# Kernel tuning notes

Hardware: AMD Instinct MI355X
Metric: run time of the kernel (lower is better)

## Reference

```python
import jax, jax.numpy as jnp
import numpy as np

N_NODES = 100000
N_EDGES = 1600000
N_PAIRS = 500000
IN_C, HID_C, OUT_C = 128, 128, 128


def setup_inputs() -> dict:
    key = jax.random.key(0)
    ks = jax.random.split(key, 12)
    def lin(k, fan_in, shape):
        b = 1.0 / np.sqrt(fan_in)
        return jax.random.uniform(k, shape, jnp.float32, -b, b)
    return {
        "x": jax.random.normal(ks[0], (N_NODES, IN_C), jnp.float32),
        "edge_index": jax.random.randint(ks[1], (2, N_EDGES), 0, N_NODES),
        "edge_pairs": jax.random.randint(ks[2], (2, N_PAIRS), 0, N_NODES),
        "W1": lin(ks[3], IN_C, (IN_C, HID_C)),
        "b1": jnp.zeros((HID_C,), jnp.float32),
        "W2": lin(ks[4], HID_C, (HID_C, OUT_C)),
        "b2": jnp.zeros((OUT_C,), jnp.float32),
        "Wm1": lin(ks[5], 2 * OUT_C, (2 * OUT_C, HID_C)),
        "bm1": lin(ks[6], 2 * OUT_C, (HID_C,)),
        "Wm2": lin(ks[7], HID_C, (HID_C, 1)),
        "bm2": lin(ks[8], HID_C, (1,)),
    }


def reference(x, edge_index, edge_pairs, W1, b1, W2, b2, Wm1, bm1, Wm2, bm2):
    N = x.shape[0]
    loop = jnp.arange(N, dtype=edge_index.dtype)
    row = jnp.concatenate([edge_index[0], loop])  # source nodes (+self loops)
    col = jnp.concatenate([edge_index[1], loop])  # target nodes (+self loops)
    # symmetric GCN normalization: deg^{-1/2}[row] * deg^{-1/2}[col]
    deg = jax.ops.segment_sum(jnp.ones(col.shape, x.dtype), col, num_segments=N)
    dinv = jnp.where(deg > 0, jax.lax.rsqrt(deg), 0.0)
    norm = dinv[row] * dinv[col]  # [E+N]

    def gcn_conv(h, W, b):
        h = h @ W  # transform first (PyG GCNConv lin has no bias)
        msg = h[row] * norm[:, None]
        return jax.ops.segment_sum(msg, col, num_segments=N) + b

    h = jax.nn.relu(gcn_conv(x, W1, b1))
    h = gcn_conv(h, W2, b2)  # dropout p=0.0 -> identity

    src, dst = edge_pairs[0], edge_pairs[1]
    ef = jnp.concatenate([h[src], h[dst]], axis=-1)  # [P, 2*out]
    out = jax.nn.relu(ef @ Wm1 + bm1) @ Wm2 + bm2
    return out.squeeze(-1)
```

## Files before the change

kernel.cpp:

```cpp
#include <hip/hip_runtime.h>
#include <hip/hip_fp16.h>

#define NCH 128
#define G_NODES 256
#define EPB 4096
#define RCAP 4864
#define MAXNB 512
#define KST 40

typedef __attribute__((ext_vector_type(8))) short short8;
typedef _Float16 half8 __attribute__((ext_vector_type(8)));
typedef __attribute__((ext_vector_type(4))) float floatx4;

static inline size_t align256(size_t x){ return (x + 255) & ~(size_t)255; }

__global__ __launch_bounds__(256) void binA_kernel(
    const int* __restrict__ row, const int* __restrict__ col,
    int* __restrict__ gcur, unsigned* __restrict__ bucketed, int E, int NB){
  __shared__ int cnt[MAXNB];
  __shared__ int lbase[MAXNB];
  __shared__ int gbase[MAXNB];
  __shared__ unsigned sorted[EPB];
  __shared__ unsigned short binOf[EPB];
  __shared__ int sh[256];
  __shared__ int carry;
  int t = threadIdx.x;
  int e0 = blockIdx.x * EPB;
  int ecnt = min(EPB, E - e0);
  for (int i = t; i < NB; i += 256) cnt[i] = 0;
  if (t == 0) carry = 0;
  __syncthreads();
  unsigned rec[16]; int bn[16]; int rk[16];
  #pragma unroll
  for (int i = 0; i < 16; i++){
    int e = e0 + i * 256 + t;
    if (e < E){
      int r = row[e], c = col[e];
      bn[i]  = c >> 8;
      rec[i] = (unsigned)r | ((unsigned)(c & 255) << 17);
      rk[i]  = atomicAdd(&cnt[bn[i]], 1);
    } else bn[i] = -1;
  }
  __syncthreads();
  for (int start = 0; start < NB; start += 256){
    int i = start + t;
    int v = (i < NB) ? cnt[i] : 0;
    sh[t] = v; __syncthreads();
    for (int off = 1; off < 256; off <<= 1){
      int val = (t >= off) ? sh[t - off] : 0;
      __syncthreads(); sh[t] += val; __syncthreads();
    }
    if (i < NB) lbase[i] = sh[t] - v + carry;
    __syncthreads();
    if (t == 255) carry += sh[255];
    __syncthreads();
  }
  for (int i = t; i < NB; i += 256){
    int c = cnt[i];
    gbase[i] = (c > 0) ? atomicAdd(&gcur[i], c) : 0;
  }
  __syncthreads();
  #pragma unroll
  for (int i = 0; i < 16; i++){
    if (bn[i] >= 0){
      int pos = lbase[bn[i]] + rk[i];
      sorted[pos] = rec[i];
      binOf[pos]  = (unsigned short)bn[i];
    }
  }
  __syncthreads();
  for (int idx = t; idx < ecnt; idx += 256){
    int b = binOf[idx];
    int gpos = gbase[b] + (idx - lbase[b]);
    if (gpos < RCAP) bucketed[(size_t)b * RCAP + gpos] = sorted[idx];
  }
}

__global__ void bscan_kernel(const int* __restrict__ gcur, int* __restrict__ bbase, int nb){
  __shared__ int sh[256];
  __shared__ int carry;
  int t = threadIdx.x;
  if (t == 0) carry = 0;
  __syncthreads();
  for (int start = 0; start < nb; start += 256){
    int i = start + t;
    int v = (i < nb) ? min(gcur[i], RCAP) : 0;
    int orig = v;
    sh[t] = v; __syncthreads();
    for (int off = 1; off < 256; off <<= 1){
      int val = (t >= off) ? sh[t - off] : 0;
      __syncthreads(); sh[t] += val; __syncthreads();
    }
    if (i < nb) bbase[i] = sh[t] - orig + carry;
    __syncthreads();
    if (t == 255) carry += sh[255];
    __syncthreads();
  }
}

__global__ __launch_bounds__(256) void binB_kernel(
    const unsigned* __restrict__ bucketed, const int* __restrict__ gcur,
    const int* __restrict__ bbase, int* __restrict__ rows_sorted,
    int* __restrict__ offs, int* __restrict__ counts, float* __restrict__ dinv, int N){
  __shared__ unsigned ledge[RCAP];
  __shared__ int cnt[G_NODES];
  __shared__ int cnt2[G_NODES];
  __shared__ int lex[G_NODES];
  __shared__ int sh[256];
  int b = blockIdx.x, t = threadIdx.x;
  int size = min(gcur[b], RCAP);
  int base = bbase[b];
  int n0 = b * G_NODES;
  cnt[t] = 0; cnt2[t] = 0;
  __syncthreads();
  for (int i = t; i < size; i += 256){
    unsigned v = bucketed[(size_t)b * RCAP + i];
    ledge[i] = v;
    atomicAdd(&cnt[v >> 17], 1);
  }
  __syncthreads();
  {
    int v = cnt[t];
    sh[t] = v; __syncthreads();
    for (int off = 1; off < 256; off <<= 1){
      int val = (t >= off) ? sh[t - off] : 0;
      __syncthreads(); sh[t] += val; __syncthreads();
    }
    lex[t] = sh[t] - v;
    int n = n0 + t;
    if (n < N){
      counts[n] = v;
      offs[n]   = base + sh[t] - v;
      dinv[n]   = rsqrtf((float)v + 1.0f);
    }
  }
  __syncthreads();
  for (int i = t; i < size; i += 256){
    unsigned v = ledge[i];
    int node = v >> 17;
    int pos = lex[node] + atomicAdd(&cnt2[node], 1);
    rows_sorted[base + pos] = (int)(v & 0x1FFFFu);
  }
}

__global__ void wprep_kernel(const float* __restrict__ W1, const float* __restrict__ W2,
                             const float* __restrict__ Wm1, short* __restrict__ planes){
  int mat = blockIdx.x >> 6;
  int idx = ((blockIdx.x & 63) << 8) + threadIdx.x;
  int k = idx >> 7, n = idx & 127;
  const float* src = (mat == 0) ? W1 : (mat == 1) ? W2 : (mat == 2) ? Wm1 : (Wm1 + 16384);
  float x = src[idx];
  short hs, ls;
  if (mat == 0){
    unsigned u = __float_as_uint(x);
    hs = (short)(u >> 16);
    float hf = __uint_as_float(u & 0xFFFF0000u);
    ls = (short)(__float_as_uint(x - hf) >> 16);
  } else {
    __half h = __float2half(x);
    __half l = __float2half(x - __half2float(h));
    hs = __half_as_short(h); ls = __half_as_short(l);
  }
  planes[(size_t)(2 * mat) * 16384 + n * 128 + k]     = hs;
  planes[(size_t)(2 * mat + 1) * 16384 + n * 128 + k] = ls;
}

__global__ __launch_bounds__(512, 4) void gemm_f32(
    const float* __restrict__ X, const short* __restrict__ Whi_,
    const short* __restrict__ Wlo_, const float* __restrict__ scale,
    __half* __restrict__ O, int nrows, int do_scale){
  __shared__ short Xhi[128 * KST];
  __shared__ short Xlo[128 * KST];
  __shared__ short Whi[128 * KST];
  __shared__ short Wlo[128 * KST];
  int t = threadIdx.x;
  int w = t >> 6, lane = t & 63;
  int m = lane & 15, q = lane >> 4;
  int row0 = blockIdx.x * 128;
  floatx4 acc[8];
  #pragma unroll
  for (int ct = 0; ct < 8; ct++) acc[ct] = (floatx4)0.f;

  for (int kc = 0; kc < 4; kc++){
    int k0 = kc * 32;
    __syncthreads();
    #pragma unroll
    for (int qq = 0; qq < 2; qq++){
      int f = t + 512 * qq;
      int r = f >> 3, kq = f & 7;
      int gr = row0 + r;
      int grc = (gr < nrows) ? gr : 0;
      float4 v = *(const float4*)(X + (size_t)grc * NCH + k0 + kq * 4);
      short h[4], l[4];
      float vv[4] = {v.x, v.y, v.z, v.w};
      #pragma unroll
      for (int j = 0; j < 4; j++){
        unsigned u = __float_as_uint(vv[j]);
        h[j] = (short)(u >> 16);
        float hf = __uint_as_float(u & 0xFFFF0000u);
        l[j] = (short)(__float_as_uint(vv[j] - hf) >> 16);
      }
      *(uint2*)(Xhi + r * KST + kq * 4) = *(uint2*)h;
      *(uint2*)(Xlo + r * KST + kq * 4) = *(uint2*)l;
    }
    {
      int n = t >> 2, kq = t & 3;
      *(uint4*)(Whi + n * KST + kq * 8) = *(const uint4*)(Whi_ + n * NCH + k0 + kq * 8);
      *(uint4*)(Wlo + n * KST + kq * 8) = *(const uint4*)(Wlo_ + n * NCH + k0 + kq * 8);
    }
    __syncthreads();
    short8 a_hi = *(const short8*)(Xhi + (w * 16 + m) * KST + q * 8);
    short8 a_lo = *(const short8*)(Xlo + (w * 16 + m) * KST + q * 8);
    #pragma unroll
    for (int ct = 0; ct < 8; ct++){
      short8 b_hi = *(const short8*)(Whi + (ct * 16 + m) * KST + q * 8);
      short8 b_lo = *(const short8*)(Wlo + (ct * 16 + m) * KST + q * 8);
      acc[ct] = __builtin_amdgcn_mfma_f32_16x16x32_bf16(a_hi, b_hi, acc[ct], 0, 0, 0);
      acc[ct] = __builtin_amdgcn_mfma_f32_16x16x32_bf16(a_lo, b_hi, acc[ct], 0, 0, 0);
      acc[ct] = __builtin_amdgcn_mfma_f32_16x16x32_bf16(a_hi, b_lo, acc[ct], 0, 0, 0);
    }
  }
  #pragma unroll
  for (int r = 0; r < 4; r++){
    int grow = row0 + w * 16 + q * 4 + r;
    if (grow < nrows){
      float sc = do_scale ? scale[grow] : 1.0f;
      #pragma unroll
      for (int ct = 0; ct < 8; ct++)
        O[(size_t)grow * NCH + ct * 16 + m] = __float2half(acc[ct][r] * sc);
    }
  }
}

template<int NCT>
__global__ __launch_bounds__(512, 4) void gemm_f16k(
    const __half* __restrict__ X,
    const short* __restrict__ Whi0, const short* __restrict__ Wlo0,
    const short* __restrict__ Whi1, const short* __restrict__ Wlo1,
    const float* __restrict__ scale,
    __half* __restrict__ O0, __half* __restrict__ O1, int nrows, int do_scale){
  __shared__ short Xs[128 * KST];
  __shared__ short Whs[NCT * 16 * KST];
  __shared__ short Wls[NCT * 16 * KST];
  int t = threadIdx.x;
  int w = t >> 6, lane = t & 63;
  int m = lane & 15, q = lane >> 4;
  int row0 = blockIdx.x * 128;
  floatx4 acc[NCT];
  #pragma unroll
  for (int ct = 0; ct < NCT; ct++) acc[ct] = (floatx4)0.f;

  for (int kc = 0; kc < 4; kc++){
    int k0 = kc * 32;
    __syncthreads();
    {
      int r = t >> 2, kq = t & 3;
      int gr = row0 + r;
      int grc = (gr < nrows) ? gr : 0;
      *(uint4*)(Xs + r * KST + kq * 8) = *(const uint4*)(X + (size_t)grc * NCH + k0 + kq * 8);
    }
    #pragma unroll
    for (int i = t; i < NCT * 16 * 4; i += 512){
      int n = i >> 2, kq = i & 3;
      const short* sh = (n < 128) ? (Whi0 + n * NCH) : (Whi1 + (n - 128) * NCH);
      const short* sl = (n < 128) ? (Wlo0 + n * NCH) : (Wlo1 + (n - 128) * NCH);
      *(uint4*)(Whs + n * KST + kq * 8) = *(const uint4*)(sh + k0 + kq * 8);
      *(uint4*)(Wls + n * KST + kq * 8) = *(const uint4*)(sl + k0 + kq * 8);
    }
    __syncthreads();
    half8 a = *(const half8*)(Xs + (w * 16 + m) * KST + q * 8);
    #pragma unroll
    for (int ct = 0; ct < NCT; ct++){
      half8 bh = *(const half8*)(Whs + (ct * 16 + m) * KST + q * 8);
      half8 bl = *(const half8*)(Wls + (ct * 16 + m) * KST + q * 8);
      acc[ct] = __builtin_amdgcn_mfma_f32_16x16x32_f16(a, bh, acc[ct], 0, 0, 0);
      acc[ct] = __builtin_amdgcn_mfma_f32_16x16x32_f16(a, bl, acc[ct], 0, 0, 0);
    }
  }
  #pragma unroll
  for (int r = 0; r < 4; r++){
    int grow = row0 + w * 16 + q * 4 + r;
    if (grow < nrows){
      float sc = do_scale ? scale[grow] : 1.0f;
      #pragma unroll
      for (int ct = 0; ct < NCT; ct++){
        __half val = __float2half(acc[ct][r] * sc);
        if (ct < 8) O0[(size_t)grow * NCH + ct * 16 + m] = val;
        else        O1[(size_t)grow * NCH + (ct - 8) * 16 + m] = val;
      }
    }
  }
}

__global__ __launch_bounds__(256) void agg_kernel(
    const __half* __restrict__ s, const float* __restrict__ dinv,
    const int* __restrict__ offs, const int* __restrict__ counts,
    const int* __restrict__ rows_sorted, const float* __restrict__ bias,
    __half* __restrict__ outp, int N, int do_relu){
  int wave = (int)((blockIdx.x * blockDim.x + threadIdx.x) >> 6);
  int lane = threadIdx.x & 63;
  if (wave >= N) return;
  int c = wave;
  int g = lane >> 4, h = lane & 15;
  float acc[8] = {0.f,0.f,0.f,0.f,0.f,0.f,0.f,0.f};
  if (g == 0){
    uint4 v = *(const uint4*)(s + (size_t)c * NCH + h * 8);
    const __half2* hp = (const __half2*)&v;
    #pragma unroll
    for (int i = 0; i < 4; i++){
      float2 f = __half22float2(hp[i]);
      acc[2*i] += f.x; acc[2*i+1] += f.y;
    }
  }
  int off = offs[c], cnt = counts[c];
  for (int chunk = 0; chunk < cnt; chunk += 64){
    int nn = min(64, cnt - chunk);
    int myidx = (lane < nn) ? rows_sorted[off + chunk + lane] : 0;
    int jmax = (nn + 3) >> 2;
    #pragma unroll 4
    for (int j = 0; j < jmax; j++){
      int e = 4 * j + g;
      int r = __shfl(myidx, e & 63, 64);
      if (e < nn){
        uint4 v = *(const uint4*)(s + (size_t)r * NCH + h * 8);
        const __half2* hp = (const __half2*)&v;
        #pragma unroll
        for (int i = 0; i < 4; i++){
          float2 f = __half22float2(hp[i]);
          acc[2*i] += f.x; acc[2*i+1] += f.y;
        }
      }
    }
  }
  #pragma unroll
  for (int i = 0; i < 8; i++){
    acc[i] += __shfl_xor(acc[i], 16, 64);
    acc[i] += __shfl_xor(acc[i], 32, 64);
  }
  if (g == 0){
    float di = dinv[c];
    float4 b0 = *(const float4*)(bias + h * 8);
    float4 b1 = *(const float4*)(bias + h * 8 + 4);
    float o[8];
    o[0] = di*acc[0]+b0.x; o[1] = di*acc[1]+b0.y; o[2] = di*acc[2]+b0.z; o[3] = di*acc[3]+b0.w;
    o[4] = di*acc[4]+b1.x; o[5] = di*acc[5]+b1.y; o[6] = di*acc[6]+b1.z; o[7] = di*acc[7]+b1.w;
    if (do_relu){
      #pragma unroll
      for (int i = 0; i < 8; i++) o[i] = fmaxf(o[i], 0.f);
    }
    __half2 packed[4];
    #pragma unroll
    for (int i = 0; i < 4; i++) packed[i] = __floats2half2_rn(o[2*i], o[2*i+1]);
    *(uint4*)(outp + (size_t)c * NCH + h * 8) = *(uint4*)packed;
  }
}

__global__ __launch_bounds__(256) void pair_kernel(
    const __half* __restrict__ A, const __half* __restrict__ B,
    const int* __restrict__ src, const int* __restrict__ dst,
    const float* __restrict__ bm1, const float* __restrict__ Wm2,
    const float* __restrict__ bm2, float* __restrict__ outp, int P){
  int gwave = (int)((blockIdx.x * blockDim.x + threadIdx.x) >> 6);
  int lane  = threadIdx.x & 63;
  int nw    = (int)((gridDim.x * blockDim.x) >> 6);
  int g = lane >> 4, h = lane & 15;
  float bb[8], ww[8];
  {
    float4 t0 = *(const float4*)(bm1 + h * 8);
    float4 t1 = *(const float4*)(bm1 + h * 8 + 4);
    bb[0]=t0.x; bb[1]=t0.y; bb[2]=t0.z; bb[3]=t0.w;
    bb[4]=t1.x; bb[5]=t1.y; bb[6]=t1.z; bb[7]=t1.w;
    float4 w0 = *(const float4*)(Wm2 + h * 8);
    float4 w1 = *(const float4*)(Wm2 + h * 8 + 4);
    ww[0]=w0.x; ww[1]=w0.y; ww[2]=w0.z; ww[3]=w0.w;
    ww[4]=w1.x; ww[5]=w1.y; ww[6]=w1.z; ww[7]=w1.w;
  }
  float bsc = bm2[0];
  const __half* basep = (g & 1) ? B : A;
  for (int p0 = gwave * 2; p0 < P; p0 += nw * 2){
    int pi = p0 + (g >> 1);
    int piX = (pi < P) ? pi : p0;
    int node = (g & 1) ? dst[piX] : src[piX];
    uint4 v = *(const uint4*)(basep + (size_t)node * NCH + h * 8);
    const __half2* hp = (const __half2*)&v;
    float f[8];
    #pragma unroll
    for (int i = 0; i < 4; i++){
      float2 t = __half22float2(hp[i]);
      f[2*i] = t.x; f[2*i+1] = t.y;
    }
    float partial = 0.f;
    #pragma unroll
    for (int i = 0; i < 8; i++){
      float other = __shfl_xor(f[i], 16, 64);
      float zi = fmaxf(f[i] + other + bb[i], 0.f);
      partial += zi * ww[i];
    }
    partial += __shfl_xor(partial, 1, 64);
    partial += __shfl_xor(partial, 2, 64);
    partial += __shfl_xor(partial, 4, 64);
    partial += __shfl_xor(partial, 8, 64);
    if ((lane & 31) == 0 && pi < P) outp[pi] = partial + bsc;
  }
}


extern "C" void kernel_launch(void* const* d_in, const int* in_sizes, int n_in,
                              void* d_out, int out_size, void* d_ws, size_t ws_size,
                              hipStream_t stream){
  const float* x   = (const float*)d_in[0];
  const int*   ei  = (const int*)  d_in[1];
  const int*   ep  = (const int*)  d_in[2];
  const float* W1  = (const float*)d_in[3];
  const float* b1  = (const float*)d_in[4];
  const float* W2  = (const float*)d_in[5];
  const float* b2  = (const float*)d_in[6];
  const float* Wm1 = (const float*)d_in[7];
  const float* bm1 = (const float*)d_in[8];
  const float* Wm2 = (const float*)d_in[9];
  const float* bm2 = (const float*)d_in[10];
  float* outp = (float*)d_out;

  const int N = in_sizes[0] / NCH;
  const int E = in_sizes[1] / 2;
  const int P = in_sizes[2] / 2;
  const int NB = (N + G_NODES - 1) / G_NODES;

  char* base = (char*)d_ws;
  size_t off = 0;
  int*      counts      = (int*)     (base + off); off = align256(off + (size_t)N * 4);
  int*      offs        = (int*)     (base + off); off = align256(off + (size_t)N * 4);
  float*    dinv        = (float*)   (base + off); off = align256(off + (size_t)N * 4);
  int*      gcur        = (int*)     (base + off); off = align256(off + (size_t)NB * 4);
  int*      bbase       = (int*)     (base + off); off = align256(off + (size_t)NB * 4);
  unsigned* bucketed    = (unsigned*)(base + off); off = align256(off + (size_t)NB * RCAP * 4);
  int*      rows_sorted = (int*)     (base + off); off = align256(off + (size_t)E * 4);
  short*    planes      = (short*)   (base + off); off = align256(off + (size_t)8 * 16384 * 2);
  __half*   sbuf        = (__half*)  (base + off); off = align256(off + (size_t)N * NCH * 2);
  __half*   hbuf        = (__half*)  (base + off); off = align256(off + (size_t)N * NCH * 2);
  __half*   sA          = (__half*)  (base + off); off = align256(off + (size_t)N * NCH * 2);
  __half*   sB          = (__half*)  (base + off); off = align256(off + (size_t)N * NCH * 2);
  (void)ws_size; (void)n_in; (void)out_size;

  short* W1hi = planes + 0 * 16384;
  short* W1lo = planes + 1 * 16384;
  short* W2hi = planes + 2 * 16384;
  short* W2lo = planes + 3 * 16384;
  short* Wahi = planes + 4 * 16384;
  short* Walo = planes + 5 * 16384;
  short* Wbhi = planes + 6 * 16384;
  short* Wblo = planes + 7 * 16384;

  const int* row = ei;
  const int* col = ei + E;
  const int* psrc = ep;
  const int* pdst = ep + P;

  hipMemsetAsync(gcur, 0, (size_t)NB * 4, stream);

  binA_kernel <<<(E + EPB - 1) / EPB, 256, 0, stream>>>(row, col, gcur, bucketed, E, NB);
  bscan_kernel<<<1, 256, 0, stream>>>(gcur, bbase, NB);
  binB_kernel <<<NB, 256, 0, stream>>>(bucketed, gcur, bbase, rows_sorted, offs, counts, dinv, N);
  wprep_kernel<<<256, 256, 0, stream>>>(W1, W2, Wm1, planes);

  int gemm_grid = (N + 127) / 128;
  int agg_grid  = (N + 3) / 4;

  gemm_f32<<<gemm_grid, 512, 0, stream>>>(x, W1hi, W1lo, dinv, sbuf, N, 1);
  agg_kernel<<<agg_grid, 256, 0, stream>>>(sbuf, dinv, offs, counts, rows_sorted, b1, hbuf, N, 1);
  gemm_f16k<8><<<gemm_grid, 512, 0, stream>>>(hbuf, W2hi, W2lo, W2hi, W2lo, dinv, sbuf, sbuf, N, 1);
  agg_kernel<<<agg_grid, 256, 0, stream>>>(sbuf, dinv, offs, counts, rows_sorted, b2, hbuf, N, 0);
  gemm_f16k<16><<<gemm_grid, 512, 0, stream>>>(hbuf, Wahi, Walo, Wbhi, Wblo, dinv, sA, sB, N, 0);
  pair_kernel<<<8192, 256, 0, stream>>>(sA, sB, psrc, pdst, bm1, Wm2, bm2, outp, P);
}
```

Measured before the change: 403.6 us.

## Store node features in 16-channel slices so gathers stay cache-local per slice

The intermediate fp16 feature buffers change from row-major [N,128] to eight channel slices of [N,16]. The GEMM kernels write and read this layout, and the aggregation and pair kernels now run one block per slice. Each slice's working set (about 3.2 MB) is small enough that random neighbor gathers can hit in L2/MALL. The cost is 32-byte gathers instead of 256-byte ones, more index and offset reloads across slices, and an extra reduction kernel that sums the per-slice pair partials.

```diff
diff --git a/kernel.cpp b/kernel.cpp
--- a/kernel.cpp
+++ b/kernel.cpp
@@ -2,6 +2,7 @@
 #include <hip/hip_fp16.h>
 
 #define NCH 128
+#define NSL 8
 #define G_NODES 256
 #define EPB 4096
 #define RCAP 4864
@@ -177,6 +178,7 @@
   int w = t >> 6, lane = t & 63;
   int m = lane & 15, q = lane >> 4;
   int row0 = blockIdx.x * 128;
+  int N = nrows;
   floatx4 acc[8];
   #pragma unroll
   for (int ct = 0; ct < 8; ct++) acc[ct] = (floatx4)0.f;
@@ -227,7 +229,7 @@
       float sc = do_scale ? scale[grow] : 1.0f;
       #pragma unroll
       for (int ct = 0; ct < 8; ct++)
-        O[(size_t)grow * NCH + ct * 16 + m] = __float2half(acc[ct][r] * sc);
+        O[((size_t)ct * N + grow) * 16 + m] = __float2half(acc[ct][r] * sc);
     }
   }
 }
@@ -246,6 +248,7 @@
   int w = t >> 6, lane = t & 63;
   int m = lane & 15, q = lane >> 4;
   int row0 = blockIdx.x * 128;
+  int N = nrows;
   floatx4 acc[NCT];
   #pragma unroll
   for (int ct = 0; ct < NCT; ct++) acc[ct] = (floatx4)0.f;
@@ -257,7 +260,10 @@
       int r = t >> 2, kq = t & 3;
       int gr = row0 + r;
       int grc = (gr < nrows) ? gr : 0;
-      *(uint4*)(Xs + r * KST + kq * 8) = *(const uint4*)(X + (size_t)grc * NCH + k0 + kq * 8);
+      int ch0 = k0 + kq * 8;
+      int sl = ch0 >> 4, within = ch0 & 15;
+      *(uint4*)(Xs + r * KST + kq * 8) =
+        *(const uint4*)(X + ((size_t)sl * N + grc) * 16 + within);
     }
     #pragma unroll
     for (int i = t; i < NCT * 16 * 4; i += 512){
@@ -285,8 +291,8 @@
       #pragma unroll
       for (int ct = 0; ct < NCT; ct++){
         __half val = __float2half(acc[ct][r] * sc);
-        if (ct < 8) O0[(size_t)grow * NCH + ct * 16 + m] = val;
-        else        O1[(size_t)grow * NCH + (ct - 8) * 16 + m] = val;
+        if (ct < 8) O0[((size_t)ct * N + grow) * 16 + m] = val;
+        else        O1[((size_t)(ct - 8) * N + grow) * 16 + m] = val;
       }
     }
   }
@@ -297,110 +303,90 @@
     const int* __restrict__ offs, const int* __restrict__ counts,
     const int* __restrict__ rows_sorted, const float* __restrict__ bias,
     __half* __restrict__ outp, int N, int do_relu){
-  int wave = (int)((blockIdx.x * blockDim.x + threadIdx.x) >> 6);
-  int lane = threadIdx.x & 63;
-  if (wave >= N) return;
-  int c = wave;
-  int g = lane >> 4, h = lane & 15;
-  float acc[8] = {0.f,0.f,0.f,0.f,0.f,0.f,0.f,0.f};
+  int slice = blockIdx.x & 7;
+  int nodeg = blockIdx.x >> 3;
+  int wavei = threadIdx.x >> 6;
+  int lane  = threadIdx.x & 63;
+  int c = nodeg * 4 + wavei;
+  if (c >= N) return;
+  int g = lane >> 3, h = lane & 7;
+  const __half* sb = s + (size_t)slice * N * 16;
+  float ax = 0.f, ay = 0.f;
   if (g == 0){
-    uint4 v = *(const uint4*)(s + (size_t)c * NCH + h * 8);
-    const __half2* hp = (const __half2*)&v;
-    #pragma unroll
-    for (int i = 0; i < 4; i++){
-      float2 f = __half22float2(hp[i]);
-      acc[2*i] += f.x; acc[2*i+1] += f.y;
-    }
+    float2 f = __half22float2(*(const __half2*)(sb + (size_t)c * 16 + 2 * h));
+    ax = f.x; ay = f.y;
   }
   int off = offs[c], cnt = counts[c];
   for (int chunk = 0; chunk < cnt; chunk += 64){
     int nn = min(64, cnt - chunk);
     int myidx = (lane < nn) ? rows_sorted[off + chunk + lane] : 0;
-    int jmax = (nn + 3) >> 2;
-    #pragma unroll 4
+    int jmax = (nn + 7) >> 3;
+    #pragma unroll 2
     for (int j = 0; j < jmax; j++){
-      int e = 4 * j + g;
+      int e = 8 * j + g;
       int r = __shfl(myidx, e & 63, 64);
       if (e < nn){
-        uint4 v = *(const uint4*)(s + (size_t)r * NCH + h * 8);
-        const __half2* hp = (const __half2*)&v;
-        #pragma unroll
-        for (int i = 0; i < 4; i++){
-          float2 f = __half22float2(hp[i]);
-          acc[2*i] += f.x; acc[2*i+1] += f.y;
-        }
+        float2 f = __half22float2(*(const __half2*)(sb + (size_t)r * 16 + 2 * h));
+        ax += f.x; ay += f.y;
       }
     }
   }
-  #pragma unroll
-  for (int i = 0; i < 8; i++){
-    acc[i] += __shfl_xor(acc[i], 16, 64);
-    acc[i] += __shfl_xor(acc[i], 32, 64);
-  }
+  ax += __shfl_xor(ax, 8, 64);  ay += __shfl_xor(ay, 8, 64);
+  ax += __shfl_xor(ax, 16, 64); ay += __shfl_xor(ay, 16, 64);
+  ax += __shfl_xor(ax, 32, 64); ay += __shfl_xor(ay, 32, 64);
   if (g == 0){
     float di = dinv[c];
-    float4 b0 = *(const float4*)(bias + h * 8);
-    float4 b1 = *(const float4*)(bias + h * 8 + 4);
-    float o[8];
-    o[0] = di*acc[0]+b0.x; o[1] = di*acc[1]+b0.y; o[2] = di*acc[2]+b0.z; o[3] = di*acc[3]+b0.w;
-    o[4] = di*acc[4]+b1.x; o[5] = di*acc[5]+b1.y; o[6] = di*acc[6]+b1.z; o[7] = di*acc[7]+b1.w;
-    if (do_relu){
-      #pragma unroll
-      for (int i = 0; i < 8; i++) o[i] = fmaxf(o[i], 0.f);
-    }
-    __half2 packed[4];
-    #pragma unroll
-    for (int i = 0; i < 4; i++) packed[i] = __floats2half2_rn(o[2*i], o[2*i+1]);
-    *(uint4*)(outp + (size_t)c * NCH + h * 8) = *(uint4*)packed;
-  }
-}
-
-__global__ __launch_bounds__(256) void pair_kernel(
+    float2 bv = *(const float2*)(bias + slice * 16 + 2 * h);
+    float ox = di * ax + bv.x;
+    float oy = di * ay + bv.y;
+    if (do_relu){ ox = fmaxf(ox, 0.f); oy = fmaxf(oy, 0.f); }
+    *(__half2*)(outp + ((size_t)slice * N + c) * 16 + 2 * h) = __floats2half2_rn(ox, oy);
+  }
+}
+
+__global__ __launch_bounds__(256) void pairp_kernel(
     const __half* __restrict__ A, const __half* __restrict__ B,
     const int* __restrict__ src, const int* __restrict__ dst,
     const float* __restrict__ bm1, const float* __restrict__ Wm2,
-    const float* __restrict__ bm2, float* __restrict__ outp, int P){
-  int gwave = (int)((blockIdx.x * blockDim.x + threadIdx.x) >> 6);
+    float* __restrict__ partials, int P, int N){
+  int slice = blockIdx.x & 7;
+  int bgrp  = blockIdx.x >> 3;
+  int nbg   = gridDim.x >> 3;
+  int wavei = threadIdx.x >> 6;
   int lane  = threadIdx.x & 63;
-  int nw    = (int)((gridDim.x * blockDim.x) >> 6);
-  int g = lane >> 4, h = lane & 15;
-  float bb[8], ww[8];
-  {
-    float4 t0 = *(const float4*)(bm1 + h * 8);
-    float4 t1 = *(const float4*)(bm1 + h * 8 + 4);
-    bb[0]=t0.x; bb[1]=t0.y; bb[2]=t0.z; bb[3]=t0.w;
-    bb[4]=t1.x; bb[5]=t1.y; bb[6]=t1.z; bb[7]=t1.w;
-    float4 w0 = *(const float4*)(Wm2 + h * 8);
-    float4 w1 = *(const float4*)(Wm2 + h * 8 + 4);
-    ww[0]=w0.x; ww[1]=w0.y; ww[2]=w0.z; ww[3]=w0.w;
-    ww[4]=w1.x; ww[5]=w1.y; ww[6]=w1.z; ww[7]=w1.w;
-  }
-  float bsc = bm2[0];
-  const __half* basep = (g & 1) ? B : A;
-  for (int p0 = gwave * 2; p0 < P; p0 += nw * 2){
-    int pi = p0 + (g >> 1);
-    int piX = (pi < P) ? pi : p0;
-    int node = (g & 1) ? dst[piX] : src[piX];
-    uint4 v = *(const uint4*)(basep + (size_t)node * NCH + h * 8);
-    const __half2* hp = (const __half2*)&v;
-    float f[8];
-    #pragma unroll
-    for (int i = 0; i < 4; i++){
-      float2 t = __half22float2(hp[i]);
-      f[2*i] = t.x; f[2*i+1] = t.y;
-    }
-    float partial = 0.f;
-    #pragma unroll
-    for (int i = 0; i < 8; i++){
-      float other = __shfl_xor(f[i], 16, 64);
-      float zi = fmaxf(f[i] + other + bb[i], 0.f);
-      partial += zi * ww[i];
-    }
+  int pr = lane >> 4, sub = lane & 15;
+  int isB = sub >> 3, hh = sub & 7;
+  int ch = slice * 16 + 2 * hh;
+  float2 bb = make_float2(bm1[ch], bm1[ch + 1]);
+  float2 ww = make_float2(Wm2[ch], Wm2[ch + 1]);
+  const __half* basep = isB ? (B + (size_t)slice * N * 16) : (A + (size_t)slice * N * 16);
+  float* pout = partials + (size_t)slice * P;
+  for (int p0 = (bgrp * 4 + wavei) * 4; p0 < P; p0 += nbg * 16){
+    int pi = p0 + pr;
+    int piX = (pi < P) ? pi : P - 1;
+    int node = isB ? dst[piX] : src[piX];
+    float2 f = __half22float2(*(const __half2*)(basep + (size_t)node * 16 + 2 * hh));
+    float ox = __shfl_xor(f.x, 8, 64);
+    float oy = __shfl_xor(f.y, 8, 64);
+    float z0 = fmaxf(f.x + ox + bb.x, 0.f);
+    float z1 = fmaxf(f.y + oy + bb.y, 0.f);
+    float partial = z0 * ww.x + z1 * ww.y;
     partial += __shfl_xor(partial, 1, 64);
     partial += __shfl_xor(partial, 2, 64);
     partial += __shfl_xor(partial, 4, 64);
-    partial += __shfl_xor(partial, 8, 64);
-    if ((lane & 31) == 0 && pi < P) outp[pi] = partial + bsc;
+    if (sub == 0 && pi < P) pout[pi] = partial;
+  }
+}
+
+__global__ void pairr_kernel(const float* __restrict__ partials,
+                             const float* __restrict__ bm2,
+                             float* __restrict__ outp, int P){
+  int p = blockIdx.x * blockDim.x + threadIdx.x;
+  if (p < P){
+    float v = bm2[0];
+    #pragma unroll
+    for (int s = 0; s < NSL; s++) v += partials[(size_t)s * P + p];
+    outp[p] = v;
   }
 }
 
@@ -440,6 +426,7 @@
   __half*   hbuf        = (__half*)  (base + off); off = align256(off + (size_t)N * NCH * 2);
   __half*   sA          = (__half*)  (base + off); off = align256(off + (size_t)N * NCH * 2);
   __half*   sB          = (__half*)  (base + off); off = align256(off + (size_t)N * NCH * 2);
+  float*    partials    = (float*)   (base + off); off = align256(off + (size_t)NSL * P * 4);
   (void)ws_size; (void)n_in; (void)out_size;
 
   short* W1hi = planes + 0 * 16384;
@@ -464,12 +451,13 @@
   wprep_kernel<<<256, 256, 0, stream>>>(W1, W2, Wm1, planes);
 
   int gemm_grid = (N + 127) / 128;
-  int agg_grid  = (N + 3) / 4;
+  int agg_grid  = 8 * ((N + 3) / 4);
 
   gemm_f32<<<gemm_grid, 512, 0, stream>>>(x, W1hi, W1lo, dinv, sbuf, N, 1);
   agg_kernel<<<agg_grid, 256, 0, stream>>>(sbuf, dinv, offs, counts, rows_sorted, b1, hbuf, N, 1);
   gemm_f16k<8><<<gemm_grid, 512, 0, stream>>>(hbuf, W2hi, W2lo, W2hi, W2lo, dinv, sbuf, sbuf, N, 1);
   agg_kernel<<<agg_grid, 256, 0, stream>>>(sbuf, dinv, offs, counts, rows_sorted, b2, hbuf, N, 0);
   gemm_f16k<16><<<gemm_grid, 512, 0, stream>>>(hbuf, Wahi, Walo, Wbhi, Wblo, dinv, sA, sB, N, 0);
-  pair_kernel<<<8192, 256, 0, stream>>>(sA, sB, psrc, pdst, bm1, Wm2, bm2, outp, P);
-}
+  pairp_kernel<<<16384, 256, 0, stream>>>(sA, sB, psrc, pdst, bm1, Wm2, partials, P, N);
+  pairr_kernel<<<(P + 255) / 256, 256, 0, stream>>>(partials, bm2, outp, P);
+}
```

Result: slower. 829.4 us (+105.5%).

## Fuse neighbor aggregation into the following GEMM kernel via shared memory

Applied to the files above, without the earlier changes.

Each GCN aggregation is merged into the next GEMM kernel. A block of 8 waves first gathers and sums neighbor features for its 128 rows, adding bias and ReLU, and writes the fp16 rows into shared memory. It then runs the MFMA GEMM straight from that tile. This removes a kernel launch and the global write and reread of the intermediate hidden features. The cost is that each wave now handles 16 nodes serially, giving less latency-hiding parallelism in the gather phase. Larger shared-memory use also lowers occupancy (launch bounds go from 4 to 2 blocks).

```diff
diff --git a/kernel.cpp b/kernel.cpp
--- a/kernel.cpp
+++ b/kernel.cpp
@@ -7,6 +7,7 @@
 #define RCAP 4864
 #define MAXNB 512
 #define KST 40
+#define XST 136
 
 typedef __attribute__((ext_vector_type(8))) short short8;
 typedef _Float16 half8 __attribute__((ext_vector_type(8)));
@@ -233,32 +234,96 @@
 }
 
 template<int NCT>
-__global__ __launch_bounds__(512, 4) void gemm_f16k(
-    const __half* __restrict__ X,
+__global__ __launch_bounds__(512, 2) void agg_gemm(
+    const __half* __restrict__ s, const float* __restrict__ dinv,
+    const int* __restrict__ offs, const int* __restrict__ counts,
+    const int* __restrict__ rows_sorted, const float* __restrict__ bias,
+    int do_relu,
     const short* __restrict__ Whi0, const short* __restrict__ Wlo0,
     const short* __restrict__ Whi1, const short* __restrict__ Wlo1,
-    const float* __restrict__ scale,
-    __half* __restrict__ O0, __half* __restrict__ O1, int nrows, int do_scale){
-  __shared__ short Xs[128 * KST];
+    const float* __restrict__ scale, int do_scale,
+    __half* __restrict__ O0, __half* __restrict__ O1, int nrows){
+  __shared__ short Xs[128 * XST];
   __shared__ short Whs[NCT * 16 * KST];
   __shared__ short Wls[NCT * 16 * KST];
   int t = threadIdx.x;
   int w = t >> 6, lane = t & 63;
+  int row0 = blockIdx.x * 128;
+
+  {
+    int g = lane >> 4, h = lane & 15;
+    for (int i = 0; i < 16; i++){
+      int local = w * 16 + i;
+      int c = row0 + local;
+      float acc[8] = {0.f,0.f,0.f,0.f,0.f,0.f,0.f,0.f};
+      if (c < nrows){
+        if (g == 0){
+          uint4 v = *(const uint4*)(s + (size_t)c * NCH + h * 8);
+          const __half2* hp = (const __half2*)&v;
+          #pragma unroll
+          for (int k = 0; k < 4; k++){
+            float2 f = __half22float2(hp[k]);
+            acc[2*k] += f.x; acc[2*k+1] += f.y;
+          }
+        }
+        int off = offs[c], cnt = counts[c];
+        for (int chunk = 0; chunk < cnt; chunk += 64){
+          int nn = min(64, cnt - chunk);
+          int myidx = (lane < nn) ? rows_sorted[off + chunk + lane] : 0;
+          int jmax = (nn + 3) >> 2;
+          #pragma unroll 4
+          for (int j = 0; j < jmax; j++){
+            int e = 4 * j + g;
+            int r = __shfl(myidx, e & 63, 64);
+            if (e < nn){
+              uint4 v = *(const uint4*)(s + (size_t)r * NCH + h * 8);
+              const __half2* hp = (const __half2*)&v;
+              #pragma unroll
+              for (int k = 0; k < 4; k++){
+                float2 f = __half22float2(hp[k]);
+                acc[2*k] += f.x; acc[2*k+1] += f.y;
+              }
+            }
+          }
+        }
+      }
+      #pragma unroll
+      for (int k = 0; k < 8; k++){
+        acc[k] += __shfl_xor(acc[k], 16, 64);
+        acc[k] += __shfl_xor(acc[k], 32, 64);
+      }
+      if (g == 0){
+        __half2 packed[4];
+        if (c < nrows){
+          float di = dinv[c];
+          float4 b0 = *(const float4*)(bias + h * 8);
+          float4 b1 = *(const float4*)(bias + h * 8 + 4);
+          float o[8];
+          o[0]=di*acc[0]+b0.x; o[1]=di*acc[1]+b0.y; o[2]=di*acc[2]+b0.z; o[3]=di*acc[3]+b0.w;
+          o[4]=di*acc[4]+b1.x; o[5]=di*acc[5]+b1.y; o[6]=di*acc[6]+b1.z; o[7]=di*acc[7]+b1.w;
+          if (do_relu){
+            #pragma unroll
+            for (int k = 0; k < 8; k++) o[k] = fmaxf(o[k], 0.f);
+          }
+          #pragma unroll
+          for (int k = 0; k < 4; k++) packed[k] = __floats2half2_rn(o[2*k], o[2*k+1]);
+        } else {
+          #pragma unroll
+          for (int k = 0; k < 4; k++) packed[k] = __floats2half2_rn(0.f, 0.f);
+        }
+        *(uint4*)(Xs + local * XST + h * 8) = *(uint4*)packed;
+      }
+    }
+  }
+
   int m = lane & 15, q = lane >> 4;
-  int row0 = blockIdx.x * 128;
-  floatx4 acc[NCT];
-  #pragma unroll
-  for (int ct = 0; ct < NCT; ct++) acc[ct] = (floatx4)0.f;
+  floatx4 acc2[NCT];
+  #pragma unroll
+  for (int ct = 0; ct < NCT; ct++) acc2[ct] = (floatx4)0.f;
 
   for (int kc = 0; kc < 4; kc++){
     int k0 = kc * 32;
     __syncthreads();
-    {
-      int r = t >> 2, kq = t & 3;
-      int gr = row0 + r;
-      int grc = (gr < nrows) ? gr : 0;
-      *(uint4*)(Xs + r * KST + kq * 8) = *(const uint4*)(X + (size_t)grc * NCH + k0 + kq * 8);
-    }
     #pragma unroll
     for (int i = t; i < NCT * 16 * 4; i += 512){
       int n = i >> 2, kq = i & 3;
@@ -268,13 +333,13 @@
       *(uint4*)(Wls + n * KST + kq * 8) = *(const uint4*)(sl + k0 + kq * 8);
     }
     __syncthreads();
-    half8 a = *(const half8*)(Xs + (w * 16 + m) * KST + q * 8);
+    half8 a = *(const half8*)(Xs + (w * 16 + m) * XST + k0 + q * 8);
     #pragma unroll
     for (int ct = 0; ct < NCT; ct++){
       half8 bh = *(const half8*)(Whs + (ct * 16 + m) * KST + q * 8);
       half8 bl = *(const half8*)(Wls + (ct * 16 + m) * KST + q * 8);
-      acc[ct] = __builtin_amdgcn_mfma_f32_16x16x32_f16(a, bh, acc[ct], 0, 0, 0);
-      acc[ct] = __builtin_amdgcn_mfma_f32_16x16x32_f16(a, bl, acc[ct], 0, 0, 0);
+      acc2[ct] = __builtin_amdgcn_mfma_f32_16x16x32_f16(a, bh, acc2[ct], 0, 0, 0);
+      acc2[ct] = __builtin_amdgcn_mfma_f32_16x16x32_f16(a, bl, acc2[ct], 0, 0, 0);
     }
   }
   #pragma unroll
@@ -284,74 +349,11 @@
       float sc = do_scale ? scale[grow] : 1.0f;
       #pragma unroll
       for (int ct = 0; ct < NCT; ct++){
-        __half val = __float2half(acc[ct][r] * sc);
+        __half val = __float2half(acc2[ct][r] * sc);
         if (ct < 8) O0[(size_t)grow * NCH + ct * 16 + m] = val;
         else        O1[(size_t)grow * NCH + (ct - 8) * 16 + m] = val;
       }
     }
-  }
-}
-
-__global__ __launch_bounds__(256) void agg_kernel(
-    const __half* __restrict__ s, const float* __restrict__ dinv,
-    const int* __restrict__ offs, const int* __restrict__ counts,
-    const int* __restrict__ rows_sorted, const float* __restrict__ bias,
-    __half* __restrict__ outp, int N, int do_relu){
-  int wave = (int)((blockIdx.x * blockDim.x + threadIdx.x) >> 6);
-  int lane = threadIdx.x & 63;
-  if (wave >= N) return;
-  int c = wave;
-  int g = lane >> 4, h = lane & 15;
-  float acc[8] = {0.f,0.f,0.f,0.f,0.f,0.f,0.f,0.f};
-  if (g == 0){
-    uint4 v = *(const uint4*)(s + (size_t)c * NCH + h * 8);
-    const __half2* hp = (const __half2*)&v;
-    #pragma unroll
-    for (int i = 0; i < 4; i++){
-      float2 f = __half22float2(hp[i]);
-      acc[2*i] += f.x; acc[2*i+1] += f.y;
-    }
-  }
-  int off = offs[c], cnt = counts[c];
-  for (int chunk = 0; chunk < cnt; chunk += 64){
-    int nn = min(64, cnt - chunk);
-    int myidx = (lane < nn) ? rows_sorted[off + chunk + lane] : 0;
-    int jmax = (nn + 3) >> 2;
-    #pragma unroll 4
-    for (int j = 0; j < jmax; j++){
-      int e = 4 * j + g;
-      int r = __shfl(myidx, e & 63, 64);
-      if (e < nn){
-        uint4 v = *(const uint4*)(s + (size_t)r * NCH + h * 8);
-        const __half2* hp = (const __half2*)&v;
-        #pragma unroll
-        for (int i = 0; i < 4; i++){
-          float2 f = __half22float2(hp[i]);
-          acc[2*i] += f.x; acc[2*i+1] += f.y;
-        }
-      }
-    }
-  }
-  #pragma unroll
-  for (int i = 0; i < 8; i++){
-    acc[i] += __shfl_xor(acc[i], 16, 64);
-    acc[i] += __shfl_xor(acc[i], 32, 64);
-  }
-  if (g == 0){
-    float di = dinv[c];
-    float4 b0 = *(const float4*)(bias + h * 8);
-    float4 b1 = *(const float4*)(bias + h * 8 + 4);
-    float o[8];
-    o[0] = di*acc[0]+b0.x; o[1] = di*acc[1]+b0.y; o[2] = di*acc[2]+b0.z; o[3] = di*acc[3]+b0.w;
-    o[4] = di*acc[4]+b1.x; o[5] = di*acc[5]+b1.y; o[6] = di*acc[6]+b1.z; o[7] = di*acc[7]+b1.w;
-    if (do_relu){
-      #pragma unroll
-      for (int i = 0; i < 8; i++) o[i] = fmaxf(o[i], 0.f);
-    }
-    __half2 packed[4];
-    #pragma unroll
-    for (int i = 0; i < 4; i++) packed[i] = __floats2half2_rn(o[2*i], o[2*i+1]);
-    *(uint4*)(outp + (size_t)c * NCH + h * 8) = *(uint4*)packed;
   }
 }
 
@@ -386,8 +388,8 @@
     float f[8];
     #pragma unroll
     for (int i = 0; i < 4; i++){
-      float2 t = __half22float2(hp[i]);
-      f[2*i] = t.x; f[2*i+1] = t.y;
+      float2 t2 = __half22float2(hp[i]);
+      f[2*i] = t2.x; f[2*i+1] = t2.y;
     }
     float partial = 0.f;
     #pragma unroll
@@ -436,8 +438,8 @@
   unsigned* bucketed    = (unsigned*)(base + off); off = align256(off + (size_t)NB * RCAP * 4);
   int*      rows_sorted = (int*)     (base + off); off = align256(off + (size_t)E * 4);
   short*    planes      = (short*)   (base + off); off = align256(off + (size_t)8 * 16384 * 2);
-  __half*   sbuf        = (__half*)  (base + off); off = align256(off + (size_t)N * NCH * 2);
-  __half*   hbuf        = (__half*)  (base + off); off = align256(off + (size_t)N * NCH * 2);
+  __half*   s1buf       = (__half*)  (base + off); off = align256(off + (size_t)N * NCH * 2);
+  __half*   s2buf       = (__half*)  (base + off); off = align256(off + (size_t)N * NCH * 2);
   __half*   sA          = (__half*)  (base + off); off = align256(off + (size_t)N * NCH * 2);
   __half*   sB          = (__half*)  (base + off); off = align256(off + (size_t)N * NCH * 2);
   (void)ws_size; (void)n_in; (void)out_size;
@@ -464,12 +466,11 @@
   wprep_kernel<<<256, 256, 0, stream>>>(W1, W2, Wm1, planes);
 
   int gemm_grid = (N + 127) / 128;
-  int agg_grid  = (N + 3) / 4;
-
-  gemm_f32<<<gemm_grid, 512, 0, stream>>>(x, W1hi, W1lo, dinv, sbuf, N, 1);
-  agg_kernel<<<agg_grid, 256, 0, stream>>>(sbuf, dinv, offs, counts, rows_sorted, b1, hbuf, N, 1);
-  gemm_f16k<8><<<gemm_grid, 512, 0, stream>>>(hbuf, W2hi, W2lo, W2hi, W2lo, dinv, sbuf, sbuf, N, 1);
-  agg_kernel<<<agg_grid, 256, 0, stream>>>(sbuf, dinv, offs, counts, rows_sorted, b2, hbuf, N, 0);
-  gemm_f16k<16><<<gemm_grid, 512, 0, stream>>>(hbuf, Wahi, Walo, Wbhi, Wblo, dinv, sA, sB, N, 0);
+
+  gemm_f32<<<gemm_grid, 512, 0, stream>>>(x, W1hi, W1lo, dinv, s1buf, N, 1);
+  agg_gemm<8><<<gemm_grid, 512, 0, stream>>>(s1buf, dinv, offs, counts, rows_sorted, b1, 1,
+                                             W2hi, W2lo, W2hi, W2lo, dinv, 1, s2buf, s2buf, N);
+  agg_gemm<16><<<gemm_grid, 512, 0, stream>>>(s2buf, dinv, offs, counts, rows_sorted, b2, 0,
+                                              Wahi, Walo, Wbhi, Wblo, dinv, 0, sA, sB, N);
   pair_kernel<<<8192, 256, 0, stream>>>(sA, sB, psrc, pdst, bm1, Wm2, bm2, outp, P);
 }
```

New measurement: 500.1 us. 1.24x slower.

## Fuse binB into first GEMM and move source scaling into aggregation

Applied to the files above, without the earlier changes.

Removes the global bucket scan by giving each bucket a fixed RCAP-stride region of rows_sorted. binB then runs as extra blocks inside the first GEMM launch, so the GEMM no longer depends on dinv. The per-source dinv scaling moves out of the GEMM epilogues into the aggregation kernel, which adds a gathered dinv load per neighbor. The memset is folded into wprep, saving launches, at the cost of a larger rows_sorted buffer and an extra scattered read in aggregation.

```diff
diff --git a/kernel.cpp b/kernel.cpp
--- a/kernel.cpp
+++ b/kernel.cpp
@@ -76,75 +76,13 @@
   }
 }
 
-__global__ void bscan_kernel(const int* __restrict__ gcur, int* __restrict__ bbase, int nb){
-  __shared__ int sh[256];
-  __shared__ int carry;
-  int t = threadIdx.x;
-  if (t == 0) carry = 0;
-  __syncthreads();
-  for (int start = 0; start < nb; start += 256){
-    int i = start + t;
-    int v = (i < nb) ? min(gcur[i], RCAP) : 0;
-    int orig = v;
-    sh[t] = v; __syncthreads();
-    for (int off = 1; off < 256; off <<= 1){
-      int val = (t >= off) ? sh[t - off] : 0;
-      __syncthreads(); sh[t] += val; __syncthreads();
-    }
-    if (i < nb) bbase[i] = sh[t] - orig + carry;
-    __syncthreads();
-    if (t == 255) carry += sh[255];
-    __syncthreads();
-  }
-}
-
-__global__ __launch_bounds__(256) void binB_kernel(
-    const unsigned* __restrict__ bucketed, const int* __restrict__ gcur,
-    const int* __restrict__ bbase, int* __restrict__ rows_sorted,
-    int* __restrict__ offs, int* __restrict__ counts, float* __restrict__ dinv, int N){
-  __shared__ unsigned ledge[RCAP];
-  __shared__ int cnt[G_NODES];
-  __shared__ int cnt2[G_NODES];
-  __shared__ int lex[G_NODES];
-  __shared__ int sh[256];
-  int b = blockIdx.x, t = threadIdx.x;
-  int size = min(gcur[b], RCAP);
-  int base = bbase[b];
-  int n0 = b * G_NODES;
-  cnt[t] = 0; cnt2[t] = 0;
-  __syncthreads();
-  for (int i = t; i < size; i += 256){
-    unsigned v = bucketed[(size_t)b * RCAP + i];
-    ledge[i] = v;
-    atomicAdd(&cnt[v >> 17], 1);
-  }
-  __syncthreads();
-  {
-    int v = cnt[t];
-    sh[t] = v; __syncthreads();
-    for (int off = 1; off < 256; off <<= 1){
-      int val = (t >= off) ? sh[t - off] : 0;
-      __syncthreads(); sh[t] += val; __syncthreads();
-    }
-    lex[t] = sh[t] - v;
-    int n = n0 + t;
-    if (n < N){
-      counts[n] = v;
-      offs[n]   = base + sh[t] - v;
-      dinv[n]   = rsqrtf((float)v + 1.0f);
-    }
-  }
-  __syncthreads();
-  for (int i = t; i < size; i += 256){
-    unsigned v = ledge[i];
-    int node = v >> 17;
-    int pos = lex[node] + atomicAdd(&cnt2[node], 1);
-    rows_sorted[base + pos] = (int)(v & 0x1FFFFu);
-  }
-}
-
 __global__ void wprep_kernel(const float* __restrict__ W1, const float* __restrict__ W2,
-                             const float* __restrict__ Wm1, short* __restrict__ planes){
+                             const float* __restrict__ Wm1, short* __restrict__ planes,
+                             int* __restrict__ gcur, int NB){
+  if (blockIdx.x < 2){
+    int i = blockIdx.x * 256 + threadIdx.x;
+    if (i < NB) gcur[i] = 0;
+  }
   int mat = blockIdx.x >> 6;
   int idx = ((blockIdx.x & 63) << 8) + threadIdx.x;
   int k = idx >> 7, n = idx & 127;
@@ -165,69 +103,116 @@
   planes[(size_t)(2 * mat + 1) * 16384 + n * 128 + k] = ls;
 }
 
-__global__ __launch_bounds__(512, 4) void gemm_f32(
+__global__ __launch_bounds__(512, 3) void fused_gemm_binB(
     const float* __restrict__ X, const short* __restrict__ Whi_,
-    const short* __restrict__ Wlo_, const float* __restrict__ scale,
-    __half* __restrict__ O, int nrows, int do_scale){
-  __shared__ short Xhi[128 * KST];
-  __shared__ short Xlo[128 * KST];
-  __shared__ short Whi[128 * KST];
-  __shared__ short Wlo[128 * KST];
+    const short* __restrict__ Wlo_, __half* __restrict__ O, int nrows, int gemmBlocks,
+    const unsigned* __restrict__ bucketed, const int* __restrict__ gcur,
+    int* __restrict__ rows_sorted, int* __restrict__ offs,
+    int* __restrict__ counts, float* __restrict__ dinv, int N){
+  __shared__ __align__(16) char smem[40960];
   int t = threadIdx.x;
-  int w = t >> 6, lane = t & 63;
-  int m = lane & 15, q = lane >> 4;
-  int row0 = blockIdx.x * 128;
-  floatx4 acc[8];
-  #pragma unroll
-  for (int ct = 0; ct < 8; ct++) acc[ct] = (floatx4)0.f;
-
-  for (int kc = 0; kc < 4; kc++){
-    int k0 = kc * 32;
-    __syncthreads();
-    #pragma unroll
-    for (int qq = 0; qq < 2; qq++){
-      int f = t + 512 * qq;
-      int r = f >> 3, kq = f & 7;
-      int gr = row0 + r;
-      int grc = (gr < nrows) ? gr : 0;
-      float4 v = *(const float4*)(X + (size_t)grc * NCH + k0 + kq * 4);
-      short h[4], l[4];
-      float vv[4] = {v.x, v.y, v.z, v.w};
+  if (blockIdx.x < gemmBlocks){
+    short* Xhi = (short*)smem;
+    short* Xlo = Xhi + 128 * KST;
+    short* Whi = Xlo + 128 * KST;
+    short* Wlo = Whi + 128 * KST;
+    int w = t >> 6, lane = t & 63;
+    int m = lane & 15, q = lane >> 4;
+    int row0 = blockIdx.x * 128;
+    floatx4 acc[8];
+    #pragma unroll
+    for (int ct = 0; ct < 8; ct++) acc[ct] = (floatx4)0.f;
+    for (int kc = 0; kc < 4; kc++){
+      int k0 = kc * 32;
+      __syncthreads();
       #pragma unroll
-      for (int j = 0; j < 4; j++){
-        unsigned u = __float_as_uint(vv[j]);
-        h[j] = (short)(u >> 16);
-        float hf = __uint_as_float(u & 0xFFFF0000u);
-        l[j] = (short)(__float_as_uint(vv[j] - hf) >> 16);
-      }
-      *(uint2*)(Xhi + r * KST + kq * 4) = *(uint2*)h;
-      *(uint2*)(Xlo + r * KST + kq * 4) = *(uint2*)l;
-    }
+      for (int qq = 0; qq < 2; qq++){
+        int f = t + 512 * qq;
+        int r = f >> 3, kq = f & 7;
+        int gr = row0 + r;
+        int grc = (gr < nrows) ? gr : 0;
+        float4 v = *(const float4*)(X + (size_t)grc * NCH + k0 + kq * 4);
+        short h[4], l[4];
+        float vv[4] = {v.x, v.y, v.z, v.w};
+        #pragma unroll
+        for (int j = 0; j < 4; j++){
+          unsigned u = __float_as_uint(vv[j]);
+          h[j] = (short)(u >> 16);
+          float hf = __uint_as_float(u & 0xFFFF0000u);
+          l[j] = (short)(__float_as_uint(vv[j] - hf) >> 16);
+        }
+        *(uint2*)(Xhi + r * KST + kq * 4) = *(uint2*)h;
+        *(uint2*)(Xlo + r * KST + kq * 4) = *(uint2*)l;
+      }
+      {
+        int n = t >> 2, kq = t & 3;
+        *(uint4*)(Whi + n * KST + kq * 8) = *(const uint4*)(Whi_ + n * NCH + k0 + kq * 8);
+        *(uint4*)(Wlo + n * KST + kq * 8) = *(const uint4*)(Wlo_ + n * NCH + k0 + kq * 8);
+      }
+      __syncthreads();
+      short8 a_hi = *(const short8*)(Xhi + (w * 16 + m) * KST + q * 8);
+      short8 a_lo = *(const short8*)(Xlo + (w * 16 + m) * KST + q * 8);
+      #pragma unroll
+      for (int ct = 0; ct < 8; ct++){
+        short8 b_hi = *(const short8*)(Whi + (ct * 16 + m) * KST + q * 8);
+        short8 b_lo = *(const short8*)(Wlo + (ct * 16 + m) * KST + q * 8);
+        acc[ct] = __builtin_amdgcn_mfma_f32_16x16x32_bf16(a_hi, b_hi, acc[ct], 0, 0, 0);
+        acc[ct] = __builtin_amdgcn_mfma_f32_16x16x32_bf16(a_lo, b_hi, acc[ct], 0, 0, 0);
+        acc[ct] = __builtin_amdgcn_mfma_f32_16x16x32_bf16(a_hi, b_lo, acc[ct], 0, 0, 0);
+      }
+    }
+    #pragma unroll
+    for (int r = 0; r < 4; r++){
+      int grow = row0 + w * 16 + q * 4 + r;
+      if (grow < nrows){
+        #pragma unroll
+        for (int ct = 0; ct < 8; ct++)
+          O[(size_t)grow * NCH + ct * 16 + m] = __float2half(acc[ct][r]);
+      }
+    }
+  } else {
+    int b = blockIdx.x - gemmBlocks;
+    unsigned* ledge = (unsigned*)smem;
+    int* cnt  = (int*)(smem + RCAP * 4);
+    int* cnt2 = cnt + 256;
+    int* lex  = cnt2 + 256;
+    int* sh   = lex + 256;
+    int size = min(gcur[b], RCAP);
+    int n0 = b * G_NODES;
+    if (t < 256){ cnt[t] = 0; cnt2[t] = 0; }
+    __syncthreads();
+    for (int i = t; i < size; i += 512){
+      unsigned v = bucketed[(size_t)b * RCAP + i];
+      ledge[i] = v;
+      atomicAdd(&cnt[v >> 17], 1);
+    }
+    __syncthreads();
     {
-      int n = t >> 2, kq = t & 3;
-      *(uint4*)(Whi + n * KST + kq * 8) = *(const uint4*)(Whi_ + n * NCH + k0 + kq * 8);
-      *(uint4*)(Wlo + n * KST + kq * 8) = *(const uint4*)(Wlo_ + n * NCH + k0 + kq * 8);
-    }
-    __syncthreads();
-    short8 a_hi = *(const short8*)(Xhi + (w * 16 + m) * KST + q * 8);
-    short8 a_lo = *(const short8*)(Xlo + (w * 16 + m) * KST + q * 8);
-    #pragma unroll
-    for (int ct = 0; ct < 8; ct++){
-      short8 b_hi = *(const short8*)(Whi + (ct * 16 + m) * KST + q * 8);
-      short8 b_lo = *(const short8*)(Wlo + (ct * 16 + m) * KST + q * 8);
-      acc[ct] = __builtin_amdgcn_mfma_f32_16x16x32_bf16(a_hi, b_hi, acc[ct], 0, 0, 0);
-      acc[ct] = __builtin_amdgcn_mfma_f32_16x16x32_bf16(a_lo, b_hi, acc[ct], 0, 0, 0);
-      acc[ct] = __builtin_amdgcn_mfma_f32_16x16x32_bf16(a_hi, b_lo, acc[ct], 0, 0, 0);
-    }
-  }
-  #pragma unroll
-  for (int r = 0; r < 4; r++){
-    int grow = row0 + w * 16 + q * 4 + r;
-    if (grow < nrows){
-      float sc = do_scale ? scale[grow] : 1.0f;
-      #pragma unroll
-      for (int ct = 0; ct < 8; ct++)
-        O[(size_t)grow * NCH + ct * 16 + m] = __float2half(acc[ct][r] * sc);
+      int v = (t < 256) ? cnt[t] : 0;
+      if (t < 256) sh[t] = v;
+      __syncthreads();
+      for (int off = 1; off < 256; off <<= 1){
+        int val = (t >= off && t < 256) ? sh[t - off] : 0;
+        __syncthreads();
+        if (t < 256) sh[t] += val;
+        __syncthreads();
+      }
+      if (t < 256){
+        lex[t] = sh[t] - v;
+        int n = n0 + t;
+        if (n < N){
+          counts[n] = v;
+          offs[n]   = b * RCAP + sh[t] - v;
+          dinv[n]   = rsqrtf((float)v + 1.0f);
+        }
+      }
+    }
+    __syncthreads();
+    for (int i = t; i < size; i += 512){
+      unsigned v = ledge[i];
+      int node = v >> 17;
+      int pos = lex[node] + atomicAdd(&cnt2[node], 1);
+      rows_sorted[(size_t)b * RCAP + pos] = (int)(v & 0x1FFFFu);
     }
   }
 }
@@ -237,8 +222,7 @@
     const __half* __restrict__ X,
     const short* __restrict__ Whi0, const short* __restrict__ Wlo0,
     const short* __restrict__ Whi1, const short* __restrict__ Wlo1,
-    const float* __restrict__ scale,
-    __half* __restrict__ O0, __half* __restrict__ O1, int nrows, int do_scale){
+    __half* __restrict__ O0, __half* __restrict__ O1, int nrows){
   __shared__ short Xs[128 * KST];
   __shared__ short Whs[NCT * 16 * KST];
   __shared__ short Wls[NCT * 16 * KST];
@@ -281,10 +265,9 @@
   for (int r = 0; r < 4; r++){
     int grow = row0 + w * 16 + q * 4 + r;
     if (grow < nrows){
-      float sc = do_scale ? scale[grow] : 1.0f;
       #pragma unroll
       for (int ct = 0; ct < NCT; ct++){
-        __half val = __float2half(acc[ct][r] * sc);
+        __half val = __float2half(acc[ct][r]);
         if (ct < 8) O0[(size_t)grow * NCH + ct * 16 + m] = val;
         else        O1[(size_t)grow * NCH + (ct - 8) * 16 + m] = val;
       }
@@ -302,6 +285,7 @@
   if (wave >= N) return;
   int c = wave;
   int g = lane >> 4, h = lane & 15;
+  float di = dinv[c];
   float acc[8] = {0.f,0.f,0.f,0.f,0.f,0.f,0.f,0.f};
   if (g == 0){
     uint4 v = *(const uint4*)(s + (size_t)c * NCH + h * 8);
@@ -309,25 +293,27 @@
     #pragma unroll
     for (int i = 0; i < 4; i++){
       float2 f = __half22float2(hp[i]);
-      acc[2*i] += f.x; acc[2*i+1] += f.y;
+      acc[2*i] = fmaf(di, f.x, acc[2*i]); acc[2*i+1] = fmaf(di, f.y, acc[2*i+1]);
     }
   }
   int off = offs[c], cnt = counts[c];
   for (int chunk = 0; chunk < cnt; chunk += 64){
     int nn = min(64, cnt - chunk);
     int myidx = (lane < nn) ? rows_sorted[off + chunk + lane] : 0;
+    float mydinv = (lane < nn) ? dinv[myidx] : 0.f;
     int jmax = (nn + 3) >> 2;
     #pragma unroll 4
     for (int j = 0; j < jmax; j++){
       int e = 4 * j + g;
-      int r = __shfl(myidx, e & 63, 64);
+      int r  = __shfl(myidx, e & 63, 64);
+      float dr = __shfl(mydinv, e & 63, 64);
       if (e < nn){
         uint4 v = *(const uint4*)(s + (size_t)r * NCH + h * 8);
         const __half2* hp = (const __half2*)&v;
         #pragma unroll
         for (int i = 0; i < 4; i++){
           float2 f = __half22float2(hp[i]);
-          acc[2*i] += f.x; acc[2*i+1] += f.y;
+          acc[2*i] = fmaf(dr, f.x, acc[2*i]); acc[2*i+1] = fmaf(dr, f.y, acc[2*i+1]);
         }
       }
     }
@@ -338,7 +324,6 @@
     acc[i] += __shfl_xor(acc[i], 32, 64);
   }
   if (g == 0){
-    float di = dinv[c];
     float4 b0 = *(const float4*)(bias + h * 8);
     float4 b1 = *(const float4*)(bias + h * 8 + 4);
     float o[8];
@@ -386,8 +371,8 @@
     float f[8];
     #pragma unroll
     for (int i = 0; i < 4; i++){
-      float2 t = __half22float2(hp[i]);
-      f[2*i] = t.x; f[2*i+1] = t.y;
+      float2 t2 = __half22float2(hp[i]);
+      f[2*i] = t2.x; f[2*i+1] = t2.y;
     }
     float partial = 0.f;
     #pragma unroll
@@ -432,12 +417,12 @@
   int*      offs        = (int*)     (base + off); off = align256(off + (size_t)N * 4);
   float*    dinv        = (float*)   (base + off); off = align256(off + (size_t)N * 4);
   int*      gcur        = (int*)     (base + off); off = align256(off + (size_t)NB * 4);
-  int*      bbase       = (int*)     (base + off); off = align256(off + (size_t)NB * 4);
   unsigned* bucketed    = (unsigned*)(base + off); off = align256(off + (size_t)NB * RCAP * 4);
-  int*      rows_sorted = (int*)     (base + off); off = align256(off + (size_t)E * 4);
+  int*      rows_sorted = (int*)     (base + off); off = align256(off + (size_t)NB * RCAP * 4);
   short*    planes      = (short*)   (base + off); off = align256(off + (size_t)8 * 16384 * 2);
-  __half*   sbuf        = (__half*)  (base + off); off = align256(off + (size_t)N * NCH * 2);
-  __half*   hbuf        = (__half*)  (base + off); off = align256(off + (size_t)N * NCH * 2);
+  __half*   s1buf       = (__half*)  (base + off); off = align256(off + (size_t)N * NCH * 2);
+  __half*   h1buf       = (__half*)  (base + off); off = align256(off + (size_t)N * NCH * 2);
+  __half*   s2buf       = (__half*)  (base + off); off = align256(off + (size_t)N * NCH * 2);
   __half*   sA          = (__half*)  (base + off); off = align256(off + (size_t)N * NCH * 2);
   __half*   sB          = (__half*)  (base + off); off = align256(off + (size_t)N * NCH * 2);
   (void)ws_size; (void)n_in; (void)out_size;
@@ -456,20 +441,17 @@
   const int* psrc = ep;
   const int* pdst = ep + P;
 
-  hipMemsetAsync(gcur, 0, (size_t)NB * 4, stream);
-
-  binA_kernel <<<(E + EPB - 1) / EPB, 256, 0, stream>>>(row, col, gcur, bucketed, E, NB);
-  bscan_kernel<<<1, 256, 0, stream>>>(gcur, bbase, NB);
-  binB_kernel <<<NB, 256, 0, stream>>>(bucketed, gcur, bbase, rows_sorted, offs, counts, dinv, N);
-  wprep_kernel<<<256, 256, 0, stream>>>(W1, W2, Wm1, planes);
-
   int gemm_grid = (N + 127) / 128;
   int agg_grid  = (N + 3) / 4;
 
-  gemm_f32<<<gemm_grid, 512, 0, stream>>>(x, W1hi, W1lo, dinv, sbuf, N, 1);
-  agg_kernel<<<agg_grid, 256, 0, stream>>>(sbuf, dinv, offs, counts, rows_sorted, b1, hbuf, N, 1);
-  gemm_f16k<8><<<gemm_grid, 512, 0, stream>>>(hbuf, W2hi, W2lo, W2hi, W2lo, dinv, sbuf, sbuf, N, 1);
-  agg_kernel<<<agg_grid, 256, 0, stream>>>(sbuf, dinv, offs, counts, rows_sorted, b2, hbuf, N, 0);
-  gemm_f16k<16><<<gemm_grid, 512, 0, stream>>>(hbuf, Wahi, Walo, Wbhi, Wblo, dinv, sA, sB, N, 0);
+  wprep_kernel<<<256, 256, 0, stream>>>(W1, W2, Wm1, planes, gcur, NB);
+  binA_kernel<<<(E + EPB - 1) / EPB, 256, 0, stream>>>(row, col, gcur, bucketed, E, NB);
+  fused_gemm_binB<<<gemm_grid + NB, 512, 0, stream>>>(
+      x, W1hi, W1lo, s1buf, N, gemm_grid,
+      bucketed, gcur, rows_sorted, offs, counts, dinv, N);
+  agg_kernel<<<agg_grid, 256, 0, stream>>>(s1buf, dinv, offs, counts, rows_sorted, b1, h1buf, N, 1);
+  gemm_f16k<8><<<gemm_grid, 512, 0, stream>>>(h1buf, W2hi, W2lo, W2hi, W2lo, s2buf, s2buf, N);
+  agg_kernel<<<agg_grid, 256, 0, stream>>>(s2buf, dinv, offs, counts, rows_sorted, b2, h1buf, N, 0);
+  gemm_f16k<16><<<gemm_grid, 512, 0, stream>>>(h1buf, Wahi, Walo, Wbhi, Wblo, sA, sB, N);
   pair_kernel<<<8192, 256, 0, stream>>>(sA, sB, psrc, pdst, bm1, Wm2, bm2, outp, P);
 }
```

Result: faster. 395.3 us (-2.1%).
